# Performance work log

Hardware: AMD Instinct MI355X
Metric: run time of the kernel (lower is better)

The kernel has to match this reference:

```python
import jax, jax.numpy as jnp
import numpy as np

BLOCK, HALO, HEADS = 8, 3, 4
WIN = BLOCK + 2 * HALO  # 14


def setup_inputs() -> dict:
    key = jax.random.key(0)
    k1, k2, k3, k4 = jax.random.split(key, 4)
    B, C, H, W = 4, 64, 192, 192
    d = C // HEADS
    return {
        "x": jax.random.normal(k1, (B, C, H, W), dtype=jnp.float32),
        "w_qkv": jax.random.normal(k2, (3 * C, C), dtype=jnp.float32) * 0.05,
        "rel_h": jax.random.normal(k3, (1, WIN, 1, d // 2), dtype=jnp.float32),
        "rel_w": jax.random.normal(k4, (1, 1, WIN, d // 2), dtype=jnp.float32),
    }


def _unfold_halo(t, nh, nw):
    B, C = t.shape[0], t.shape[1]
    tp = jnp.pad(t, ((0, 0), (0, 0), (HALO, HALO), (HALO, HALO)))
    ri = (jnp.arange(nh) * BLOCK)[:, None] + jnp.arange(WIN)
    ci = (jnp.arange(nw) * BLOCK)[:, None] + jnp.arange(WIN)
    p = tp[:, :, ri, :]
    p = p[:, :, :, :, ci]
    p = p.transpose(0, 2, 4, 3, 5, 1)
    return p.reshape(B * nh * nw, WIN * WIN, C)


def reference(x, w_qkv, rel_h, rel_w):
    B, C, H, W = x.shape
    d = C // HEADS
    nh, nw = H // BLOCK, W // BLOCK
    # 1x1 conv qkv
    qkv = jnp.einsum('bchw,oc->bohw', x, w_qkv)
    q, k, v = jnp.split(qkv, 3, axis=1)
    # q -> per-block tokens: (B*nh*nw, BLOCK*BLOCK, C)
    q = q.reshape(B, C, nh, BLOCK, nw, BLOCK).transpose(0, 2, 4, 3, 5, 1)
    q = q.reshape(B * nh * nw, BLOCK * BLOCK, C) * (d ** -0.5)
    k = _unfold_halo(k, nh, nw)
    v = _unfold_halo(v, nh, nw)
    # split heads: '(b) a (h d) -> (b h) a d'
    q = q.reshape(-1, BLOCK * BLOCK, HEADS, d).transpose(0, 2, 1, 3).reshape(-1, BLOCK * BLOCK, d)
    v = v.reshape(-1, WIN * WIN, HEADS, d).transpose(0, 2, 1, 3).reshape(-1, WIN * WIN, d)
    k = k.reshape(-1, WIN, WIN, HEADS, d).transpose(0, 3, 1, 2, 4).reshape(-1, WIN, WIN, d)
    # inline relative position bias added to keys
    kh, kw = k[..., : d // 2], k[..., d // 2:]
    k = jnp.concatenate([kh + rel_h, kw + rel_w], axis=-1).reshape(-1, WIN * WIN, d)
    sim = jnp.einsum('bid,bjd->bij', q, k)          # (BLh, 64, 196)
    attn = jax.nn.softmax(sim, axis=-1)
    out = jnp.einsum('bij,bjd->bid', attn, v)       # (BLh, 64, d)
    # fold back: '(b h w n) (k1 k2) d -> b (n d) (h k1) (w k2)'
    out = out.reshape(B, nh, nw, HEADS, BLOCK, BLOCK, d)
    out = out.transpose(0, 3, 6, 1, 4, 2, 5).reshape(B, HEADS * d, nh * BLOCK, nw * BLOCK)
    return out
```

## Files before the change

### kernel.cpp

```cpp
#include <hip/hip_runtime.h>
#include <hip/hip_bf16.h>

constexpr int B = 4, C = 64, H = 192, W = 192;
constexpr int HEADS = 4, D = 16;
constexpr int BLK = 8, HALO = 3, WIN = 14;
constexpr int NH = H / BLK, NW = W / BLK;
constexpr int HW = H * W;
constexpr int O = 3 * C;

constexpr int K_ROWS = 200;
constexpr int K_OFF = 0;
constexpr int V_OFF = K_ROWS * 64;
constexpr int VPLANE = 208 * 16;
constexpr int RH_OFF = V_OFF + 4 * VPLANE;
constexpr int RW_OFF = RH_OFF + 128;
constexpr int LDS_TOT = RW_OFF + 128;

constexpr int K_ITEMS = K_ROWS * 8;
constexpr int TOT_ITEMS = K_ITEMS + 208 * 8;

typedef __attribute__((ext_vector_type(4))) short short4v;
typedef __attribute__((ext_vector_type(8))) short short8v;
typedef __attribute__((ext_vector_type(8))) __bf16 bf16x8;
typedef __attribute__((ext_vector_type(4))) float f32x4;

__device__ inline f32x4 mfma_bf16(short8v a, short8v b, f32x4 c) {
  return __builtin_amdgcn_mfma_f32_16x16x32_bf16(
      __builtin_bit_cast(bf16x8, a), __builtin_bit_cast(bf16x8, b), c, 0, 0, 0);
}

__device__ inline unsigned short f2bf(float f) {
  __bf16 h = (__bf16)f;
  return __builtin_bit_cast(unsigned short, h);
}

__device__ inline unsigned cvt_pk_bf16(float a, float b) {
  unsigned r;
  asm("v_cvt_pk_bf16_f32 %0, %1, %2" : "=v"(r) : "v"(a), "v"(b));
  return r;
}

__global__ __launch_bounds__(256) void qkv_mfma(
    const float* __restrict__ x, const float* __restrict__ w,
    unsigned short* __restrict__ qkv) {
  __shared__ unsigned short wlds[192 * 64];
  const int tid = threadIdx.x;

  const float4* wf4 = reinterpret_cast<const float4*>(w);
#pragma unroll
  for (int it = 0; it < 12; ++it) {
    const int idx = it * 256 + tid;
    const int o = idx >> 4;
    const int c = (idx & 15) << 2;
    const float4 wv = wf4[idx];
    ushort4 st;
    st.x = f2bf(wv.x);
    st.y = f2bf(wv.y);
    st.z = f2bf(wv.z);
    st.w = f2bf(wv.w);
    const int sw = (((c >> 3) ^ (o & 7)) << 3) + (c & 4);
    *reinterpret_cast<ushort4*>(&wlds[o * 64 + sw]) = st;
  }

  const int wave = tid >> 6, lane = tid & 63;
  const int p = lane & 15, g = lane >> 4;
  const int pix_w = blockIdx.x * 128 + wave * 32;
  const int b = pix_w / HW;
  const int hw = pix_w - b * HW + p;
  const float* xb = x + (size_t)b * C * HW;

  short8v xf[2][2];
#pragma unroll
  for (int pt = 0; pt < 2; ++pt) {
#pragma unroll
    for (int ks = 0; ks < 2; ++ks) {
      unsigned short u[8];
#pragma unroll
      for (int j = 0; j < 8; ++j)
        u[j] = f2bf(xb[(size_t)(ks * 32 + g * 8 + j) * HW + hw + pt * 16]);
      unsigned int pw[4];
#pragma unroll
      for (int e = 0; e < 4; ++e)
        pw[e] = (unsigned int)u[2 * e] | ((unsigned int)u[2 * e + 1] << 16);
      xf[pt][ks] = __builtin_bit_cast(short8v, *reinterpret_cast<uint4*>(pw));
    }
  }
  __syncthreads();

#pragma unroll
  for (int ot = 0; ot < 12; ++ot) {
    short8v af[2];
#pragma unroll
    for (int ks = 0; ks < 2; ++ks)
      af[ks] = *reinterpret_cast<const short8v*>(
          wlds + (ot * 16 + p) * 64 + (((((ks << 2) | g)) ^ (p & 7)) << 3));
    const float s = (ot < 4) ? 0.25f * 1.44269504f : 1.0f;
#pragma unroll
    for (int pt = 0; pt < 2; ++pt) {
      f32x4 acc = {0.f, 0.f, 0.f, 0.f};
      acc = mfma_bf16(af[0], xf[pt][0], acc);
      acc = mfma_bf16(af[1], xf[pt][1], acc);
      ushort4 st;
      st.x = f2bf(acc[0] * s);
      st.y = f2bf(acc[1] * s);
      st.z = f2bf(acc[2] * s);
      st.w = f2bf(acc[3] * s);
      *reinterpret_cast<ushort4*>(
          qkv + (size_t)(pix_w + pt * 16 + p) * O + ot * 16 + g * 4) = st;
    }
  }
}

__global__ __launch_bounds__(512, 4) void attn_kernel(
    const unsigned short* __restrict__ qkv,
    const float* __restrict__ rel_h, const float* __restrict__ rel_w,
    float* __restrict__ out) {
  __shared__ __align__(16) unsigned short lds[LDS_TOT];

  const int tid = threadIdx.x;
  const int blk = blockIdx.x;
  const int win = (blk & 7) * 288 + (blk >> 3);
  const int b = win / (NH * NW);
  const int wrem = win - b * (NH * NW);
  const int bh = wrem / NW;
  const int bw = wrem - bh * NW;
  const int y0 = bh * BLK - HALO;
  const int x0 = bw * BLK - HALO;

  if (tid < 256) {
    const int i = tid & 127;
    const int rr = i >> 3, cc = i & 7;
    const int rc = (rr < WIN) ? rr : (WIN - 1);
    const float* src = (tid < 128) ? rel_h : rel_w;
    lds[((tid < 128) ? RH_OFF : RW_OFF) + i] = f2bf(src[rc * 8 + cc]);
  }

  uint4 raw[7];
#pragma unroll
  for (int it = 0; it < 7; ++it) {
    const int item = tid + it * 512;
    const bool isK = item < K_ITEMS;
    const int li = isK ? item : item - K_ITEMS;
    const int pixel = li >> 3;
    const int g = li & 7;
    const int wy = pixel / WIN;
    const int wx = pixel - wy * WIN;
    const int y = y0 + wy, xx = x0 + wx;
    const bool inb = (item < TOT_ITEMS) & ((unsigned)y < (unsigned)H) &
                     ((unsigned)xx < (unsigned)W);
    uint4 rv = make_uint4(0u, 0u, 0u, 0u);
    if (inb)
      rv = *reinterpret_cast<const uint4*>(
          qkv + ((size_t)(b * HW + y * W + xx)) * O + (isK ? C : 2 * C) + g * 8);
    raw[it] = rv;
  }

  const int lane = tid & 63;
  const int wv = tid >> 6;
  const int head = wv & 3;
  const int qhalf = wv >> 2;
  const int r = lane & 15, hq = lane >> 4;
  const int qrow0 = qhalf * 32 + r;
  short8v qf0, qf1;
  {
    const int y = bh * BLK + (qrow0 >> 3);
    const int xx = bw * BLK + (qrow0 & 7);
    qf0 = *reinterpret_cast<const short8v*>(
        qkv + ((size_t)(b * HW + y * W + xx)) * O + head * D + (hq & 1) * 8);
    const int qrow1 = qrow0 + 16;
    const int y1 = bh * BLK + (qrow1 >> 3);
    const int xx1 = bw * BLK + (qrow1 & 7);
    qf1 = *reinterpret_cast<const short8v*>(
        qkv + ((size_t)(b * HW + y1 * W + xx1)) * O + head * D + (hq & 1) * 8);
  }

#pragma unroll
  for (int it = 0; it < 7; ++it) {
    const int item = tid + it * 512;
    if (item < TOT_ITEMS) {
      const bool isK = item < K_ITEMS;
      const int li = isK ? item : item - K_ITEMS;
      const int pixel = li >> 3;
      const int g = li & 7;
      if (isK) {
        const int ch = (g ^ pixel) & 7;
        *reinterpret_cast<uint4*>(&lds[K_OFF + pixel * 64 + ch * 8]) = raw[it];
      } else {
        const int hd = g >> 1, c8 = g & 1;
        *reinterpret_cast<uint4*>(
            &lds[V_OFF + hd * VPLANE + pixel * 16 + c8 * 8]) = raw[it];
      }
    }
  }
  __syncthreads();

  int koff[13];
#pragma unroll
  for (int t = 0; t < 13; ++t) {
    const int row = 16 * t + r;
    const int wy = row / WIN;
    const int wx = row - wy * WIN;
    const int a_k =
        K_OFF + row * 64 + ((((head << 1) | (hq & 1)) ^ (row & 7)) << 3);
    const int a_rh = RH_OFF + wy * 8;
    const int a_rw = RW_OFF + wx * 8;
    koff[t] = (hq < 2) ? a_k : ((hq == 2) ? a_rh : a_rw);
  }

  const unsigned vbase_addr =
      (unsigned)(unsigned long long)(const void*)&lds[V_OFF + head * VPLANE] +
      (unsigned)(lane * 8);
  short4v vlo[7], vhi[7];
#pragma unroll
  for (int tau = 0; tau < 7; ++tau) {
    const unsigned va = vbase_addr + tau * 1024;
    asm volatile("ds_read_b64_tr_b16 %0, %1" : "=v"(vlo[tau]) : "v"(va));
    if (tau < 6) {
      asm volatile("ds_read_b64_tr_b16 %0, %1 offset:512"
                   : "=v"(vhi[tau])
                   : "v"(va));
    } else {
      vhi[tau] = (short4v){0, 0, 0, 0};
    }
  }
  asm volatile("s_waitcnt lgkmcnt(0)" ::: "memory");
  __builtin_amdgcn_sched_barrier(0);

  __builtin_amdgcn_s_setprio(1);

  f32x4 oacc0 = {0.f, 0.f, 0.f, 0.f}, oacc1 = {0.f, 0.f, 0.f, 0.f};
  float sum0 = 0.f, sum1 = 0.f;
#pragma unroll
  for (int tau = 0; tau < 7; ++tau) {
    unsigned pw0[4], pw1[4];
#pragma unroll
    for (int half = 0; half < 2; ++half) {
      const int t = 2 * tau + half;
      if (t < 13) {
        const short8v kf = *reinterpret_cast<const short8v*>(&lds[koff[t]]);
        const f32x4 z4 = {0.f, 0.f, 0.f, 0.f};
        const f32x4 s0 = mfma_bf16(kf, qf0, z4);
        const f32x4 s1 = mfma_bf16(kf, qf1, z4);
        float p0e[4], p1e[4];
#pragma unroll
        for (int e = 0; e < 4; ++e) {
          float pa = __builtin_amdgcn_exp2f(s0[e]);
          float pb = __builtin_amdgcn_exp2f(s1[e]);
          if (t == 12 && hq >= 1) {
            pa = 0.f;
            pb = 0.f;
          }
          sum0 += pa;
          sum1 += pb;
          p0e[e] = pa;
          p1e[e] = pb;
        }
        pw0[half * 2 + 0] = cvt_pk_bf16(p0e[0], p0e[1]);
        pw0[half * 2 + 1] = cvt_pk_bf16(p0e[2], p0e[3]);
        pw1[half * 2 + 0] = cvt_pk_bf16(p1e[0], p1e[1]);
        pw1[half * 2 + 1] = cvt_pk_bf16(p1e[2], p1e[3]);
      } else {
        pw0[2] = 0u;
        pw0[3] = 0u;
        pw1[2] = 0u;
        pw1[3] = 0u;
      }
    }
    const short8v vf =
        __builtin_shufflevector(vlo[tau], vhi[tau], 0, 1, 2, 3, 4, 5, 6, 7);
    const uint4 u0 = make_uint4(pw0[0], pw0[1], pw0[2], pw0[3]);
    const uint4 u1 = make_uint4(pw1[0], pw1[1], pw1[2], pw1[3]);
    oacc0 = mfma_bf16(vf, __builtin_bit_cast(short8v, u0), oacc0);
    oacc1 = mfma_bf16(vf, __builtin_bit_cast(short8v, u1), oacc1);
  }

  sum0 += __shfl_xor(sum0, 16);
  sum0 += __shfl_xor(sum0, 32);
  sum1 += __shfl_xor(sum1, 16);
  sum1 += __shfl_xor(sum1, 32);
  const float inv0 = 1.f / sum0;
  const float inv1 = 1.f / sum1;

  {
    const int y = bh * BLK + (qrow0 >> 3);
    const int xx = bw * BLK + (qrow0 & 7);
    float* op = out + ((size_t)b * C + head * D + 4 * hq) * HW + y * W + xx;
#pragma unroll
    for (int e = 0; e < 4; ++e) op[(size_t)e * HW] = oacc0[e] * inv0;
  }
  {
    const int qrow1 = qrow0 + 16;
    const int y = bh * BLK + (qrow1 >> 3);
    const int xx = bw * BLK + (qrow1 & 7);
    float* op = out + ((size_t)b * C + head * D + 4 * hq) * HW + y * W + xx;
#pragma unroll
    for (int e = 0; e < 4; ++e) op[(size_t)e * HW] = oacc1[e] * inv1;
  }
  __builtin_amdgcn_s_setprio(0);
}

extern "C" void kernel_launch(void* const* d_in, const int* in_sizes, int n_in,
                              void* d_out, int out_size, void* d_ws,
                              size_t ws_size, hipStream_t stream) {
  const float* x = (const float*)d_in[0];
  const float* w_qkv = (const float*)d_in[1];
  const float* rel_h = (const float*)d_in[2];
  const float* rel_w = (const float*)d_in[3];
  float* out = (float*)d_out;

  unsigned short* qkv = (unsigned short*)d_ws;

  qkv_mfma<<<B * HW / 128, 256, 0, stream>>>(x, w_qkv, qkv);
  attn_kernel<<<B * NH * NW, 512, 0, stream>>>(qkv, rel_h, rel_w, out);
}
```

Before: 63.47 us.

## Split attention blocks by head pair to halve per-block LDS and threads

Each attention workgroup now handles two of the four heads for a window instead of all four. The launch doubles the grid and halves the block size to 256 threads. K and V tiles in LDS shrink to the 32 channels of the head pair, with an adjusted swizzle and padded V planes, so more workgroups can be resident per CU. The trade-off is that window index math and the relative-position table loads are repeated per pair, and the halo K/V rows are fetched by two blocks.

Result: no change. 62.81 us (-1.0%).

```diff
diff --git a/kernel.cpp b/kernel.cpp
--- a/kernel.cpp
+++ b/kernel.cpp
@@ -9,15 +9,16 @@
 constexpr int O = 3 * C;
 
 constexpr int K_ROWS = 200;
+constexpr int KSTRIDE = 32;
 constexpr int K_OFF = 0;
-constexpr int V_OFF = K_ROWS * 64;
-constexpr int VPLANE = 208 * 16;
-constexpr int RH_OFF = V_OFF + 4 * VPLANE;
+constexpr int V_OFF = 6656;
+constexpr int VPLANE = 208 * 16 + 16;
+constexpr int RH_OFF = V_OFF + 2 * VPLANE;
 constexpr int RW_OFF = RH_OFF + 128;
 constexpr int LDS_TOT = RW_OFF + 128;
 
-constexpr int K_ITEMS = K_ROWS * 8;
-constexpr int TOT_ITEMS = K_ITEMS + 208 * 8;
+constexpr int K_ITEMS = K_ROWS * 4;
+constexpr int TOT_ITEMS = K_ITEMS + 208 * 4;
 
 typedef __attribute__((ext_vector_type(4))) short short4v;
 typedef __attribute__((ext_vector_type(8))) short short8v;
@@ -111,7 +112,7 @@
   }
 }
 
-__global__ __launch_bounds__(512, 4) void attn_kernel(
+__global__ __launch_bounds__(256, 4) void attn_kernel(
     const unsigned short* __restrict__ qkv,
     const float* __restrict__ rel_h, const float* __restrict__ rel_w,
     float* __restrict__ out) {
@@ -119,7 +120,9 @@
 
   const int tid = threadIdx.x;
   const int blk = blockIdx.x;
-  const int win = (blk & 7) * 288 + (blk >> 3);
+  const int hpair = blk & 1;
+  const int wr = blk >> 1;
+  const int win = (wr & 7) * 288 + (wr >> 3);
   const int b = win / (NH * NW);
   const int wrem = win - b * (NH * NW);
   const int bh = wrem / NW;
@@ -127,7 +130,7 @@
   const int y0 = bh * BLK - HALO;
   const int x0 = bw * BLK - HALO;
 
-  if (tid < 256) {
+  {
     const int i = tid & 127;
     const int rr = i >> 3, cc = i & 7;
     const int rc = (rr < WIN) ? rr : (WIN - 1);
@@ -138,11 +141,11 @@
   uint4 raw[7];
 #pragma unroll
   for (int it = 0; it < 7; ++it) {
-    const int item = tid + it * 512;
+    const int item = tid + it * 256;
     const bool isK = item < K_ITEMS;
     const int li = isK ? item : item - K_ITEMS;
-    const int pixel = li >> 3;
-    const int g = li & 7;
+    const int pixel = li >> 2;
+    const int g = li & 3;
     const int wy = pixel / WIN;
     const int wx = pixel - wy * WIN;
     const int y = y0 + wy, xx = x0 + wx;
@@ -151,14 +154,16 @@
     uint4 rv = make_uint4(0u, 0u, 0u, 0u);
     if (inb)
       rv = *reinterpret_cast<const uint4*>(
-          qkv + ((size_t)(b * HW + y * W + xx)) * O + (isK ? C : 2 * C) + g * 8);
+          qkv + ((size_t)(b * HW + y * W + xx)) * O + (isK ? C : 2 * C) +
+          (hpair << 5) + (g << 3));
     raw[it] = rv;
   }
 
   const int lane = tid & 63;
   const int wv = tid >> 6;
-  const int head = wv & 3;
-  const int qhalf = wv >> 2;
+  const int lh = wv & 1;
+  const int head = hpair * 2 + lh;
+  const int qhalf = wv >> 1;
   const int r = lane & 15, hq = lane >> 4;
   const int qrow0 = qhalf * 32 + r;
   short8v qf0, qf1;
@@ -176,19 +181,20 @@
 
 #pragma unroll
   for (int it = 0; it < 7; ++it) {
-    const int item = tid + it * 512;
+    const int item = tid + it * 256;
     if (item < TOT_ITEMS) {
       const bool isK = item < K_ITEMS;
       const int li = isK ? item : item - K_ITEMS;
-      const int pixel = li >> 3;
-      const int g = li & 7;
+      const int pixel = li >> 2;
+      const int g = li & 3;
       if (isK) {
-        const int ch = (g ^ pixel) & 7;
-        *reinterpret_cast<uint4*>(&lds[K_OFF + pixel * 64 + ch * 8]) = raw[it];
+        const int ch = (g ^ pixel) & 3;
+        *reinterpret_cast<uint4*>(&lds[K_OFF + pixel * KSTRIDE + ch * 8]) =
+            raw[it];
       } else {
-        const int hd = g >> 1, c8 = g & 1;
+        const int vlh = g >> 1, c8 = g & 1;
         *reinterpret_cast<uint4*>(
-            &lds[V_OFF + hd * VPLANE + pixel * 16 + c8 * 8]) = raw[it];
+            &lds[V_OFF + vlh * VPLANE + pixel * 16 + c8 * 8]) = raw[it];
       }
     }
   }
@@ -201,14 +207,14 @@
     const int wy = row / WIN;
     const int wx = row - wy * WIN;
     const int a_k =
-        K_OFF + row * 64 + ((((head << 1) | (hq & 1)) ^ (row & 7)) << 3);
+        K_OFF + row * KSTRIDE + (((((lh << 1) | (hq & 1)) ^ row) & 3) << 3);
     const int a_rh = RH_OFF + wy * 8;
     const int a_rw = RW_OFF + wx * 8;
     koff[t] = (hq < 2) ? a_k : ((hq == 2) ? a_rh : a_rw);
   }
 
   const unsigned vbase_addr =
-      (unsigned)(unsigned long long)(const void*)&lds[V_OFF + head * VPLANE] +
+      (unsigned)(unsigned long long)(const void*)&lds[V_OFF + lh * VPLANE] +
       (unsigned)(lane * 8);
   short4v vlo[7], vhi[7];
 #pragma unroll
@@ -311,5 +317,5 @@
   unsigned short* qkv = (unsigned short*)d_ws;
 
   qkv_mfma<<<B * HW / 128, 256, 0, stream>>>(x, w_qkv, qkv);
-  attn_kernel<<<B * NH * NW, 512, 0, stream>>>(qkv, rel_h, rel_w, out);
-}
+  attn_kernel<<<B * NH * NW * 2, 256, 0, stream>>>(qkv, rel_h, rel_w, out);
+}
```
